# Performance work log

Hardware: AMD Instinct MI355X
Metric: run time of the kernel (lower is better)

Reference implementation:

```python
import jax, jax.numpy as jnp
import numpy as np

N = 50000
E = 800000
D_IN = 128
D_HID = 256


def setup_inputs() -> dict:
    key = jax.random.key(0)
    ks = jax.random.split(key, 12)
    s = 0.02
    return {
        "node_features": jax.random.normal(ks[0], (N, D_IN), dtype=jnp.float32),
        "edge_index": jax.random.randint(ks[1], (2, E), 0, N, dtype=jnp.int64),
        # layer 0 (input_dim -> hidden)
        "eps0": jnp.zeros((), dtype=jnp.float32),
        "W1_0": jax.random.normal(ks[2], (D_IN, D_HID), dtype=jnp.float32) * s,
        "b1_0": jnp.zeros((D_HID,), dtype=jnp.float32),
        "W2_0": jax.random.normal(ks[3], (D_HID, D_HID), dtype=jnp.float32) * s,
        "b2_0": jnp.zeros((D_HID,), dtype=jnp.float32),
        # layer 1 (hidden -> hidden)
        "eps1": jnp.zeros((), dtype=jnp.float32),
        "W1_1": jax.random.normal(ks[4], (D_HID, D_HID), dtype=jnp.float32) * s,
        "b1_1": jnp.zeros((D_HID,), dtype=jnp.float32),
        "W2_1": jax.random.normal(ks[5], (D_HID, D_HID), dtype=jnp.float32) * s,
        "b2_1": jnp.zeros((D_HID,), dtype=jnp.float32),
        # fc_out (hidden -> input_dim)
        "Wo": jax.random.normal(ks[6], (D_HID, D_IN), dtype=jnp.float32) * s,
        "bo": jnp.zeros((D_IN,), dtype=jnp.float32),
    }


def _gin_layer(x, src, dst, eps, W1, b1, W2, b2):
    # gather neighbor features + scatter-add into destination nodes
    agg = jnp.zeros_like(x).at[dst].add(x[src])  # [N, d]
    h = (1.0 + eps) * x + agg
    h = jax.nn.relu(h @ W1 + b1)
    return h @ W2 + b2


def reference(node_features, edge_index, eps0, W1_0, b1_0, W2_0, b2_0,
              eps1, W1_1, b1_1, W2_1, b2_1, Wo, bo):
    src, dst = edge_index[0], edge_index[1]
    h = _gin_layer(node_features, src, dst, eps0, W1_0, b1_0, W2_0, b2_0)
    h = _gin_layer(h, src, dst, eps1, W1_1, b1_1, W2_1, b2_1)
    return h @ Wo + bo  # [N, input_dim]
```

## Files before the change

### kernel.cpp

```cpp
#include <hip/hip_runtime.h>

#define NN 50000
#define NE 800000
#define DIN 128
#define DHID 256
#define MAXDEG 128

typedef __bf16 bf16x8 __attribute__((ext_vector_type(8)));
typedef float f32x4 __attribute__((ext_vector_type(4)));

static __device__ __forceinline__ unsigned short f2bf(float f) {
    unsigned u = __float_as_uint(f);
    unsigned r = 0x7fffu + ((u >> 16) & 1u);
    return (unsigned short)((u + r) >> 16);
}
static __device__ __forceinline__ float blo(unsigned u) { return __uint_as_float(u << 16); }
static __device__ __forceinline__ float bhi(unsigned u) { return __uint_as_float(u & 0xffff0000u); }


__global__ void bucket_kernel(const int* __restrict__ src, const int* __restrict__ dst,
                              int* __restrict__ cnt, int* __restrict__ srcs, int E) {
    int i4 = (blockIdx.x * blockDim.x + threadIdx.x) * 4;
    if (i4 >= E) return;
    int4 d4 = *(const int4*)&dst[i4];
    int4 s4 = *(const int4*)&src[i4];
    int t0 = atomicAdd(&cnt[d4.x], 1);
    int t1 = atomicAdd(&cnt[d4.y], 1);
    int t2 = atomicAdd(&cnt[d4.z], 1);
    int t3 = atomicAdd(&cnt[d4.w], 1);
    if (t0 < MAXDEG) srcs[(size_t)d4.x * MAXDEG + t0] = s4.x;
    if (t1 < MAXDEG) srcs[(size_t)d4.y * MAXDEG + t1] = s4.y;
    if (t2 < MAXDEG) srcs[(size_t)d4.z * MAXDEG + t2] = s4.z;
    if (t3 < MAXDEG) srcs[(size_t)d4.w * MAXDEG + t3] = s4.w;
}


__global__ void prep_kernel(const float* __restrict__ x, unsigned short* __restrict__ xb,
                            int* __restrict__ cnt,
                            const float* __restrict__ W1_0, const float* __restrict__ W2_0,
                            const float* __restrict__ W1_1, const float* __restrict__ W2_1,
                            const float* __restrict__ Wo,
                            unsigned short* __restrict__ w10t, unsigned short* __restrict__ w20t,
                            unsigned short* __restrict__ w11t, unsigned short* __restrict__ w21t,
                            unsigned short* __restrict__ wot) {
    int i = blockIdx.x * blockDim.x + threadIdx.x;
    if (i < NN) cnt[i] = 0;
    if (i < 262144) {
        const float* W; unsigned short* Wt; int K, N, idx;
        if (i < 32768)        { W = W1_0; Wt = w10t; K = 128; N = 256; idx = i; }
        else if (i < 98304)   { W = W2_0; Wt = w20t; K = 256; N = 256; idx = i - 32768; }
        else if (i < 163840)  { W = W1_1; Wt = w11t; K = 256; N = 256; idx = i - 98304; }
        else if (i < 229376)  { W = W2_1; Wt = w21t; K = 256; N = 256; idx = i - 163840; }
        else                  { W = Wo;   Wt = wot;  K = 256; N = 128; idx = i - 229376; }
        int k = idx / N;
        int n = idx - k * N;
        Wt[(size_t)n * K + k] = f2bf(W[idx]);
    }
    if (i * 4 < NN * DIN) {
        float4 v = *(const float4*)(x + (size_t)i * 4);
        ushort4 o;
        o.x = f2bf(v.x); o.y = f2bf(v.y); o.z = f2bf(v.z); o.w = f2bf(v.w);
        *(ushort4*)(xb + (size_t)i * 4) = o;
    }
}


template <int D>
__global__ void agg_bf16_kernel(const unsigned short* __restrict__ x, const int* __restrict__ cnt,
                                const int* __restrict__ srcs, const float* __restrict__ eps_p,
                                unsigned short* __restrict__ out, int n) {
    int gtid = blockIdx.x * blockDim.x + threadIdx.x;
    int node = gtid >> 6;
    int lane = threadIdx.x & 63;
    if (node >= n) return;
    int deg = cnt[node]; if (deg > MAXDEG) deg = MAXDEG;
    const int* sp = srcs + (size_t)node * MAXDEG;
    float e = 1.0f + eps_p[0];
    if constexpr (D == 128) {
        const unsigned* xp = (const unsigned*)x;
        float a0 = 0.f, a1 = 0.f, b0 = 0.f, b1 = 0.f;
        int i = 0;
        for (; i + 8 <= deg; i += 8) {
            unsigned v[8];
            #pragma unroll
            for (int j = 0; j < 8; j++) v[j] = xp[(size_t)sp[i + j] * 64 + lane];
            #pragma unroll
            for (int j = 0; j < 8; j += 2) {
                a0 += blo(v[j]);     a1 += bhi(v[j]);
                b0 += blo(v[j + 1]); b1 += bhi(v[j + 1]);
            }
        }
        for (; i < deg; i++) {
            unsigned v = xp[(size_t)sp[i] * 64 + lane];
            a0 += blo(v); a1 += bhi(v);
        }
        unsigned xv = xp[(size_t)node * 64 + lane];
        a0 += b0 + e * blo(xv);
        a1 += b1 + e * bhi(xv);
        ((unsigned*)out)[(size_t)node * 64 + lane] =
            (unsigned)f2bf(a0) | ((unsigned)f2bf(a1) << 16);
    } else {
        const uint2* xp = (const uint2*)x;
        float a0 = 0.f, a1 = 0.f, a2 = 0.f, a3 = 0.f;
        float b0 = 0.f, b1 = 0.f, b2 = 0.f, b3 = 0.f;
        int i = 0;
        for (; i + 8 <= deg; i += 8) {
            uint2 v[8];
            #pragma unroll
            for (int j = 0; j < 8; j++) v[j] = xp[(size_t)sp[i + j] * 64 + lane];
            #pragma unroll
            for (int j = 0; j < 8; j += 2) {
                a0 += blo(v[j].x);     a1 += bhi(v[j].x);     a2 += blo(v[j].y);     a3 += bhi(v[j].y);
                b0 += blo(v[j + 1].x); b1 += bhi(v[j + 1].x); b2 += blo(v[j + 1].y); b3 += bhi(v[j + 1].y);
            }
        }
        for (; i < deg; i++) {
            uint2 v = xp[(size_t)sp[i] * 64 + lane];
            a0 += blo(v.x); a1 += bhi(v.x); a2 += blo(v.y); a3 += bhi(v.y);
        }
        uint2 xv = xp[(size_t)node * 64 + lane];
        a0 += b0 + e * blo(xv.x);
        a1 += b1 + e * bhi(xv.x);
        a2 += b2 + e * blo(xv.y);
        a3 += b3 + e * bhi(xv.y);
        uint2 o;
        o.x = (unsigned)f2bf(a0) | ((unsigned)f2bf(a1) << 16);
        o.y = (unsigned)f2bf(a2) | ((unsigned)f2bf(a3) << 16);
        ((uint2*)out)[(size_t)node * 64 + lane] = o;
    }
}


template <int K1, int THREE>
__global__ __launch_bounds__(256, 2) void mlp_fused(
        const unsigned short* __restrict__ A,
        const unsigned short* __restrict__ W1t, const float* __restrict__ b1,
        const unsigned short* __restrict__ W2t, const float* __restrict__ b2,
        const unsigned short* __restrict__ W3t, const float* __restrict__ b3,
        unsigned short* __restrict__ Cb, float* __restrict__ Cf, int M) {
    constexpr int NKS1 = K1 / 32;
    __shared__ __align__(16) unsigned short H[(THREE ? 2 : 1) * 64 * 256];
    unsigned short* H1 = H;
    unsigned short* H2 = H + 64 * 256;

    const int tid = threadIdx.x;
    const int lane = tid & 63;
    const int w = tid >> 6;
    const int quad = lane >> 4;
    const int l16 = lane & 15;
    const size_t rowbase = (size_t)blockIdx.x * 64;

    bf16x8 bfrag[8][4];
    f32x4 bvv[4];

    #pragma unroll
    for (int ks = 0; ks < NKS1; ks++)
        #pragma unroll
        for (int nt = 0; nt < 4; nt++)
            bfrag[ks][nt] = *(const bf16x8*)&W1t[(size_t)(w * 64 + nt * 16 + l16) * K1 + ks * 32 + quad * 8];
    #pragma unroll
    for (int nt = 0; nt < 4; nt++)
        bvv[nt] = *(const f32x4*)&b1[w * 64 + nt * 16 + quad * 4];

    #pragma unroll
    for (int j = 0; j < 4; j++) {
        const unsigned short* ar = A + (rowbase + j * 16 + l16) * K1 + quad * 8;
        bf16x8 af[NKS1];
        #pragma unroll
        for (int ks = 0; ks < NKS1; ks++) af[ks] = *(const bf16x8*)(ar + ks * 32);
        f32x4 acc[4];
        #pragma unroll
        for (int nt = 0; nt < 4; nt++) acc[nt] = (f32x4)(0.f);
        #pragma unroll
        for (int ks = 0; ks < NKS1; ks++)
            #pragma unroll
            for (int nt = 0; nt < 4; nt++)
                acc[nt] = __builtin_amdgcn_mfma_f32_16x16x32_bf16(bfrag[ks][nt], af[ks], acc[nt], 0, 0, 0);
        int r = j * 16 + l16;
        #pragma unroll
        for (int nt = 0; nt < 4; nt++) {
            f32x4 v = acc[nt] + bvv[nt];
            v[0] = fmaxf(v[0], 0.f); v[1] = fmaxf(v[1], 0.f);
            v[2] = fmaxf(v[2], 0.f); v[3] = fmaxf(v[3], 0.f);
            int c = w * 8 + nt * 2 + (quad >> 1);
            int cs = c ^ (r & 7);
            uint2 o;
            o.x = (unsigned)f2bf(v[0]) | ((unsigned)f2bf(v[1]) << 16);
            o.y = (unsigned)f2bf(v[2]) | ((unsigned)f2bf(v[3]) << 16);
            *(uint2*)&H1[r * 256 + cs * 8 + (quad & 1) * 4] = o;
        }
    }
    __syncthreads();

    #pragma unroll
    for (int ks = 0; ks < 8; ks++)
        #pragma unroll
        for (int nt = 0; nt < 4; nt++)
            bfrag[ks][nt] = *(const bf16x8*)&W2t[(size_t)(w * 64 + nt * 16 + l16) * 256 + ks * 32 + quad * 8];
    #pragma unroll
    for (int nt = 0; nt < 4; nt++)
        bvv[nt] = *(const f32x4*)&b2[w * 64 + nt * 16 + quad * 4];

    #pragma unroll
    for (int j = 0; j < 4; j++) {
        int r = j * 16 + l16;
        bf16x8 af[8];
        #pragma unroll
        for (int ks = 0; ks < 8; ks++) {
            int cs = (ks * 4 + quad) ^ (r & 7);
            af[ks] = *(const bf16x8*)&H1[r * 256 + cs * 8];
        }
        f32x4 acc[4];
        #pragma unroll
        for (int nt = 0; nt < 4; nt++) acc[nt] = (f32x4)(0.f);
        #pragma unroll
        for (int ks = 0; ks < 8; ks++)
            #pragma unroll
            for (int nt = 0; nt < 4; nt++)
                acc[nt] = __builtin_amdgcn_mfma_f32_16x16x32_bf16(bfrag[ks][nt], af[ks], acc[nt], 0, 0, 0);
        if constexpr (!THREE) {
            size_t gm = rowbase + j * 16 + l16;
            if (gm < (size_t)M) {
                #pragma unroll
                for (int nt = 0; nt < 4; nt++) {
                    f32x4 v = acc[nt] + bvv[nt];
                    uint2 o;
                    o.x = (unsigned)f2bf(v[0]) | ((unsigned)f2bf(v[1]) << 16);
                    o.y = (unsigned)f2bf(v[2]) | ((unsigned)f2bf(v[3]) << 16);
                    *(uint2*)&Cb[gm * 256 + w * 64 + nt * 16 + quad * 4] = o;
                }
            }
        } else {
            #pragma unroll
            for (int nt = 0; nt < 4; nt++) {
                f32x4 v = acc[nt] + bvv[nt];
                int c = w * 8 + nt * 2 + (quad >> 1);
                int cs = c ^ (r & 7);
                uint2 o;
                o.x = (unsigned)f2bf(v[0]) | ((unsigned)f2bf(v[1]) << 16);
                o.y = (unsigned)f2bf(v[2]) | ((unsigned)f2bf(v[3]) << 16);
                *(uint2*)&H2[r * 256 + cs * 8 + (quad & 1) * 4] = o;
            }
        }
    }

    if constexpr (THREE) {
        __syncthreads();
        #pragma unroll
        for (int ks = 0; ks < 8; ks++)
            #pragma unroll
            for (int nt = 0; nt < 2; nt++)
                bfrag[ks][nt] = *(const bf16x8*)&W3t[(size_t)(w * 32 + nt * 16 + l16) * 256 + ks * 32 + quad * 8];
        f32x4 bv3[2];
        #pragma unroll
        for (int nt = 0; nt < 2; nt++)
            bv3[nt] = *(const f32x4*)&b3[w * 32 + nt * 16 + quad * 4];

        #pragma unroll
        for (int j = 0; j < 4; j++) {
            int r = j * 16 + l16;
            bf16x8 af[8];
            #pragma unroll
            for (int ks = 0; ks < 8; ks++) {
                int cs = (ks * 4 + quad) ^ (r & 7);
                af[ks] = *(const bf16x8*)&H2[r * 256 + cs * 8];
            }
            f32x4 acc[2];
            #pragma unroll
            for (int nt = 0; nt < 2; nt++) acc[nt] = (f32x4)(0.f);
            #pragma unroll
            for (int ks = 0; ks < 8; ks++)
                #pragma unroll
                for (int nt = 0; nt < 2; nt++)
                    acc[nt] = __builtin_amdgcn_mfma_f32_16x16x32_bf16(bfrag[ks][nt], af[ks], acc[nt], 0, 0, 0);
            size_t gm = rowbase + j * 16 + l16;
            if (gm < (size_t)M) {
                #pragma unroll
                for (int nt = 0; nt < 2; nt++) {
                    f32x4 v = acc[nt] + bv3[nt];
                    *(f32x4*)&Cf[gm * 128 + w * 32 + nt * 16 + quad * 4] = v;
                }
            }
        }
    }
}


static inline size_t align256(size_t v) { return (v + 255) & ~(size_t)255; }

extern "C" void kernel_launch(void* const* d_in, const int* in_sizes, int n_in,
                              void* d_out, int out_size, void* d_ws, size_t ws_size,
                              hipStream_t stream) {
    const float* x        = (const float*)d_in[0];
    const int*   ei       = (const int*)d_in[1];
    const float* eps0     = (const float*)d_in[2];
    const float* W1_0     = (const float*)d_in[3];
    const float* b1_0     = (const float*)d_in[4];
    const float* W2_0     = (const float*)d_in[5];
    const float* b2_0     = (const float*)d_in[6];
    const float* eps1     = (const float*)d_in[7];
    const float* W1_1     = (const float*)d_in[8];
    const float* b1_1     = (const float*)d_in[9];
    const float* W2_1     = (const float*)d_in[10];
    const float* b2_1     = (const float*)d_in[11];
    const float* Wo       = (const float*)d_in[12];
    const float* bo       = (const float*)d_in[13];
    float* out            = (float*)d_out;

    const int* srcE = ei;
    const int* dstE = ei + NE;

    char* p = (char*)d_ws;
    size_t o = 0;
    int* cnt  = (int*)(p + o); o = align256(o + (size_t)NN * 4);
    int* srcs = (int*)(p + o); o = align256(o + (size_t)NN * MAXDEG * 4);
    unsigned short* xb   = (unsigned short*)(p + o); o = align256(o + (size_t)NN * DIN * 2);
    unsigned short* w10t = (unsigned short*)(p + o); o = align256(o + (size_t)DHID * DIN * 2);
    unsigned short* w20t = (unsigned short*)(p + o); o = align256(o + (size_t)DHID * DHID * 2);
    unsigned short* w11t = (unsigned short*)(p + o); o = align256(o + (size_t)DHID * DHID * 2);
    unsigned short* w21t = (unsigned short*)(p + o); o = align256(o + (size_t)DHID * DHID * 2);
    unsigned short* wot  = (unsigned short*)(p + o); o = align256(o + (size_t)DIN * DHID * 2);
    unsigned short* bufA = (unsigned short*)(p + o); o = align256(o + (size_t)NN * DHID * 2 + 65536);
    unsigned short* bufB = (unsigned short*)(p + o); o = align256(o + (size_t)NN * DHID * 2 + 65536);

    prep_kernel<<<(NN * DIN / 4 + 255) / 256, 256, 0, stream>>>(
        x, xb, cnt, W1_0, W2_0, W1_1, W2_1, Wo, w10t, w20t, w11t, w21t, wot);
    bucket_kernel<<<(NE / 4 + 255) / 256, 256, 0, stream>>>(srcE, dstE, cnt, srcs, NE);

    int aggBlocks = (NN * 64 + 255) / 256;
    int mlpBlocks = (NN + 63) / 64;

    agg_bf16_kernel<DIN><<<aggBlocks, 256, 0, stream>>>(xb, cnt, srcs, eps0, bufA, NN);
    mlp_fused<128, 0><<<mlpBlocks, 256, 0, stream>>>(
        bufA, w10t, b1_0, w20t, b2_0, nullptr, nullptr, bufB, nullptr, NN);

    agg_bf16_kernel<DHID><<<aggBlocks, 256, 0, stream>>>(bufB, cnt, srcs, eps1, bufA, NN);
    mlp_fused<256, 1><<<mlpBlocks, 256, 0, stream>>>(
        bufA, w11t, b1_1, w21t, b2_1, wot, bo, nullptr, out, NN);
}
```

Measured before the change: 348.2 us.

## Pack multiple nodes per wave in aggregation and restructure MLP loop order

The aggregation kernel now assigns 4 (D=128) or 2 (D=256) nodes per wave, with each lane loading 16-byte uint4 chunks and reading neighbour indices as int4. The fused MLP switches from preloading all weight fragments per layer to streaming weights per k-step into a 4x4 accumulator tile, reuses a single shared buffer for both hidden layers, and drops the occupancy hint from launch_bounds. The bucket kernel processes 8 edges per thread instead of 4. These changes aim to widen memory transactions and cut register pressure, at the cost of more lane divergence from uneven node degrees within a wave and extra barriers.

Measured after the change: 331.1 us. -4.9%, faster.

```diff
diff --git a/kernel.cpp b/kernel.cpp
--- a/kernel.cpp
+++ b/kernel.cpp
@@ -20,18 +20,28 @@
 
 __global__ void bucket_kernel(const int* __restrict__ src, const int* __restrict__ dst,
                               int* __restrict__ cnt, int* __restrict__ srcs, int E) {
-    int i4 = (blockIdx.x * blockDim.x + threadIdx.x) * 4;
-    if (i4 >= E) return;
-    int4 d4 = *(const int4*)&dst[i4];
-    int4 s4 = *(const int4*)&src[i4];
-    int t0 = atomicAdd(&cnt[d4.x], 1);
-    int t1 = atomicAdd(&cnt[d4.y], 1);
-    int t2 = atomicAdd(&cnt[d4.z], 1);
-    int t3 = atomicAdd(&cnt[d4.w], 1);
-    if (t0 < MAXDEG) srcs[(size_t)d4.x * MAXDEG + t0] = s4.x;
-    if (t1 < MAXDEG) srcs[(size_t)d4.y * MAXDEG + t1] = s4.y;
-    if (t2 < MAXDEG) srcs[(size_t)d4.z * MAXDEG + t2] = s4.z;
-    if (t3 < MAXDEG) srcs[(size_t)d4.w * MAXDEG + t3] = s4.w;
+    int i8 = (blockIdx.x * blockDim.x + threadIdx.x) * 8;
+    if (i8 >= E) return;
+    int4 da = *(const int4*)&dst[i8];
+    int4 db = *(const int4*)&dst[i8 + 4];
+    int4 sa = *(const int4*)&src[i8];
+    int4 sb = *(const int4*)&src[i8 + 4];
+    int t0 = atomicAdd(&cnt[da.x], 1);
+    int t1 = atomicAdd(&cnt[da.y], 1);
+    int t2 = atomicAdd(&cnt[da.z], 1);
+    int t3 = atomicAdd(&cnt[da.w], 1);
+    int t4 = atomicAdd(&cnt[db.x], 1);
+    int t5 = atomicAdd(&cnt[db.y], 1);
+    int t6 = atomicAdd(&cnt[db.z], 1);
+    int t7 = atomicAdd(&cnt[db.w], 1);
+    if (t0 < MAXDEG) srcs[(size_t)da.x * MAXDEG + t0] = sa.x;
+    if (t1 < MAXDEG) srcs[(size_t)da.y * MAXDEG + t1] = sa.y;
+    if (t2 < MAXDEG) srcs[(size_t)da.z * MAXDEG + t2] = sa.z;
+    if (t3 < MAXDEG) srcs[(size_t)da.w * MAXDEG + t3] = sa.w;
+    if (t4 < MAXDEG) srcs[(size_t)db.x * MAXDEG + t4] = sb.x;
+    if (t5 < MAXDEG) srcs[(size_t)db.y * MAXDEG + t5] = sb.y;
+    if (t6 < MAXDEG) srcs[(size_t)db.z * MAXDEG + t6] = sb.z;
+    if (t7 < MAXDEG) srcs[(size_t)db.w * MAXDEG + t7] = sb.w;
 }
 
 
@@ -69,215 +79,213 @@
 __global__ void agg_bf16_kernel(const unsigned short* __restrict__ x, const int* __restrict__ cnt,
                                 const int* __restrict__ srcs, const float* __restrict__ eps_p,
                                 unsigned short* __restrict__ out, int n) {
-    int gtid = blockIdx.x * blockDim.x + threadIdx.x;
-    int node = gtid >> 6;
+    constexpr int G = (D == 128) ? 4 : 2;
+    constexpr int L = 64 / G;
+    constexpr int RQ = D / 8;
+    int tid = blockIdx.x * blockDim.x + threadIdx.x;
+    int wid = tid >> 6;
     int lane = threadIdx.x & 63;
+    int group = lane / L;
+    int li = lane % L;
+    int node = wid * G + group;
     if (node >= n) return;
     int deg = cnt[node]; if (deg > MAXDEG) deg = MAXDEG;
     const int* sp = srcs + (size_t)node * MAXDEG;
+    const uint4* xp = (const uint4*)x;
     float e = 1.0f + eps_p[0];
-    if constexpr (D == 128) {
-        const unsigned* xp = (const unsigned*)x;
-        float a0 = 0.f, a1 = 0.f, b0 = 0.f, b1 = 0.f;
-        int i = 0;
-        for (; i + 8 <= deg; i += 8) {
-            unsigned v[8];
-            #pragma unroll
-            for (int j = 0; j < 8; j++) v[j] = xp[(size_t)sp[i + j] * 64 + lane];
-            #pragma unroll
-            for (int j = 0; j < 8; j += 2) {
-                a0 += blo(v[j]);     a1 += bhi(v[j]);
-                b0 += blo(v[j + 1]); b1 += bhi(v[j + 1]);
-            }
-        }
-        for (; i < deg; i++) {
-            unsigned v = xp[(size_t)sp[i] * 64 + lane];
-            a0 += blo(v); a1 += bhi(v);
-        }
-        unsigned xv = xp[(size_t)node * 64 + lane];
-        a0 += b0 + e * blo(xv);
-        a1 += b1 + e * bhi(xv);
-        ((unsigned*)out)[(size_t)node * 64 + lane] =
-            (unsigned)f2bf(a0) | ((unsigned)f2bf(a1) << 16);
-    } else {
-        const uint2* xp = (const uint2*)x;
-        float a0 = 0.f, a1 = 0.f, a2 = 0.f, a3 = 0.f;
-        float b0 = 0.f, b1 = 0.f, b2 = 0.f, b3 = 0.f;
-        int i = 0;
-        for (; i + 8 <= deg; i += 8) {
-            uint2 v[8];
-            #pragma unroll
-            for (int j = 0; j < 8; j++) v[j] = xp[(size_t)sp[i + j] * 64 + lane];
-            #pragma unroll
-            for (int j = 0; j < 8; j += 2) {
-                a0 += blo(v[j].x);     a1 += bhi(v[j].x);     a2 += blo(v[j].y);     a3 += bhi(v[j].y);
-                b0 += blo(v[j + 1].x); b1 += bhi(v[j + 1].x); b2 += blo(v[j + 1].y); b3 += bhi(v[j + 1].y);
-            }
-        }
-        for (; i < deg; i++) {
-            uint2 v = xp[(size_t)sp[i] * 64 + lane];
-            a0 += blo(v.x); a1 += bhi(v.x); a2 += blo(v.y); a3 += bhi(v.y);
-        }
-        uint2 xv = xp[(size_t)node * 64 + lane];
-        a0 += b0 + e * blo(xv.x);
-        a1 += b1 + e * bhi(xv.x);
-        a2 += b2 + e * blo(xv.y);
-        a3 += b3 + e * bhi(xv.y);
-        uint2 o;
-        o.x = (unsigned)f2bf(a0) | ((unsigned)f2bf(a1) << 16);
-        o.y = (unsigned)f2bf(a2) | ((unsigned)f2bf(a3) << 16);
-        ((uint2*)out)[(size_t)node * 64 + lane] = o;
-    }
+
+    float a[8], b[8];
+    #pragma unroll
+    for (int j = 0; j < 8; j++) { a[j] = 0.f; b[j] = 0.f; }
+
+    int i = 0;
+    for (; i + 4 <= deg; i += 4) {
+        int4 s = *(const int4*)&sp[i];
+        uint4 v0 = xp[(size_t)s.x * RQ + li];
+        uint4 v1 = xp[(size_t)s.y * RQ + li];
+        uint4 v2 = xp[(size_t)s.z * RQ + li];
+        uint4 v3 = xp[(size_t)s.w * RQ + li];
+        a[0] += blo(v0.x); a[1] += bhi(v0.x); a[2] += blo(v0.y); a[3] += bhi(v0.y);
+        a[4] += blo(v0.z); a[5] += bhi(v0.z); a[6] += blo(v0.w); a[7] += bhi(v0.w);
+        b[0] += blo(v1.x); b[1] += bhi(v1.x); b[2] += blo(v1.y); b[3] += bhi(v1.y);
+        b[4] += blo(v1.z); b[5] += bhi(v1.z); b[6] += blo(v1.w); b[7] += bhi(v1.w);
+        a[0] += blo(v2.x); a[1] += bhi(v2.x); a[2] += blo(v2.y); a[3] += bhi(v2.y);
+        a[4] += blo(v2.z); a[5] += bhi(v2.z); a[6] += blo(v2.w); a[7] += bhi(v2.w);
+        b[0] += blo(v3.x); b[1] += bhi(v3.x); b[2] += blo(v3.y); b[3] += bhi(v3.y);
+        b[4] += blo(v3.z); b[5] += bhi(v3.z); b[6] += blo(v3.w); b[7] += bhi(v3.w);
+    }
+    for (; i < deg; i++) {
+        uint4 v = xp[(size_t)sp[i] * RQ + li];
+        a[0] += blo(v.x); a[1] += bhi(v.x); a[2] += blo(v.y); a[3] += bhi(v.y);
+        a[4] += blo(v.z); a[5] += bhi(v.z); a[6] += blo(v.w); a[7] += bhi(v.w);
+    }
+    uint4 xv = xp[(size_t)node * RQ + li];
+    a[0] += b[0] + e * blo(xv.x); a[1] += b[1] + e * bhi(xv.x);
+    a[2] += b[2] + e * blo(xv.y); a[3] += b[3] + e * bhi(xv.y);
+    a[4] += b[4] + e * blo(xv.z); a[5] += b[5] + e * bhi(xv.z);
+    a[6] += b[6] + e * blo(xv.w); a[7] += b[7] + e * bhi(xv.w);
+    uint4 o;
+    o.x = (unsigned)f2bf(a[0]) | ((unsigned)f2bf(a[1]) << 16);
+    o.y = (unsigned)f2bf(a[2]) | ((unsigned)f2bf(a[3]) << 16);
+    o.z = (unsigned)f2bf(a[4]) | ((unsigned)f2bf(a[5]) << 16);
+    o.w = (unsigned)f2bf(a[6]) | ((unsigned)f2bf(a[7]) << 16);
+    ((uint4*)out)[(size_t)node * RQ + li] = o;
 }
 
 
 template <int K1, int THREE>
-__global__ __launch_bounds__(256, 2) void mlp_fused(
+__global__ __launch_bounds__(256) void mlp_fused(
         const unsigned short* __restrict__ A,
         const unsigned short* __restrict__ W1t, const float* __restrict__ b1,
         const unsigned short* __restrict__ W2t, const float* __restrict__ b2,
         const unsigned short* __restrict__ W3t, const float* __restrict__ b3,
         unsigned short* __restrict__ Cb, float* __restrict__ Cf, int M) {
     constexpr int NKS1 = K1 / 32;
-    __shared__ __align__(16) unsigned short H[(THREE ? 2 : 1) * 64 * 256];
-    unsigned short* H1 = H;
-    unsigned short* H2 = H + 64 * 256;
-
-    const int tid = threadIdx.x;
-    const int lane = tid & 63;
-    const int w = tid >> 6;
+    __shared__ __align__(16) unsigned short H[64 * 256];
+
+    const int lane = threadIdx.x & 63;
+    const int w = threadIdx.x >> 6;
     const int quad = lane >> 4;
     const int l16 = lane & 15;
     const size_t rowbase = (size_t)blockIdx.x * 64;
 
-    bf16x8 bfrag[8][4];
-    f32x4 bvv[4];
+    f32x4 acc[4][4];
 
     #pragma unroll
-    for (int ks = 0; ks < NKS1; ks++)
+    for (int j = 0; j < 4; j++)
+        #pragma unroll
+        for (int nt = 0; nt < 4; nt++) acc[j][nt] = (f32x4)(0.f);
+    #pragma unroll 2
+    for (int ks = 0; ks < NKS1; ks++) {
+        bf16x8 bw[4];
         #pragma unroll
         for (int nt = 0; nt < 4; nt++)
-            bfrag[ks][nt] = *(const bf16x8*)&W1t[(size_t)(w * 64 + nt * 16 + l16) * K1 + ks * 32 + quad * 8];
-    #pragma unroll
-    for (int nt = 0; nt < 4; nt++)
-        bvv[nt] = *(const f32x4*)&b1[w * 64 + nt * 16 + quad * 4];
-
-    #pragma unroll
-    for (int j = 0; j < 4; j++) {
-        const unsigned short* ar = A + (rowbase + j * 16 + l16) * K1 + quad * 8;
-        bf16x8 af[NKS1];
-        #pragma unroll
-        for (int ks = 0; ks < NKS1; ks++) af[ks] = *(const bf16x8*)(ar + ks * 32);
-        f32x4 acc[4];
-        #pragma unroll
-        for (int nt = 0; nt < 4; nt++) acc[nt] = (f32x4)(0.f);
-        #pragma unroll
-        for (int ks = 0; ks < NKS1; ks++)
+            bw[nt] = *(const bf16x8*)&W1t[(size_t)(w * 64 + nt * 16 + l16) * K1 + ks * 32 + quad * 8];
+        #pragma unroll
+        for (int j = 0; j < 4; j++) {
+            bf16x8 af = *(const bf16x8*)&A[(rowbase + j * 16 + l16) * K1 + ks * 32 + quad * 8];
             #pragma unroll
             for (int nt = 0; nt < 4; nt++)
-                acc[nt] = __builtin_amdgcn_mfma_f32_16x16x32_bf16(bfrag[ks][nt], af[ks], acc[nt], 0, 0, 0);
-        int r = j * 16 + l16;
-        #pragma unroll
-        for (int nt = 0; nt < 4; nt++) {
-            f32x4 v = acc[nt] + bvv[nt];
-            v[0] = fmaxf(v[0], 0.f); v[1] = fmaxf(v[1], 0.f);
-            v[2] = fmaxf(v[2], 0.f); v[3] = fmaxf(v[3], 0.f);
-            int c = w * 8 + nt * 2 + (quad >> 1);
-            int cs = c ^ (r & 7);
-            uint2 o;
-            o.x = (unsigned)f2bf(v[0]) | ((unsigned)f2bf(v[1]) << 16);
-            o.y = (unsigned)f2bf(v[2]) | ((unsigned)f2bf(v[3]) << 16);
-            *(uint2*)&H1[r * 256 + cs * 8 + (quad & 1) * 4] = o;
-        }
-    }
-    __syncthreads();
-
-    #pragma unroll
-    for (int ks = 0; ks < 8; ks++)
+                acc[j][nt] = __builtin_amdgcn_mfma_f32_16x16x32_bf16(bw[nt], af, acc[j][nt], 0, 0, 0);
+        }
+    }
+    {
+        f32x4 bvv[4];
         #pragma unroll
         for (int nt = 0; nt < 4; nt++)
-            bfrag[ks][nt] = *(const bf16x8*)&W2t[(size_t)(w * 64 + nt * 16 + l16) * 256 + ks * 32 + quad * 8];
-    #pragma unroll
-    for (int nt = 0; nt < 4; nt++)
-        bvv[nt] = *(const f32x4*)&b2[w * 64 + nt * 16 + quad * 4];
-
-    #pragma unroll
-    for (int j = 0; j < 4; j++) {
-        int r = j * 16 + l16;
-        bf16x8 af[8];
-        #pragma unroll
-        for (int ks = 0; ks < 8; ks++) {
-            int cs = (ks * 4 + quad) ^ (r & 7);
-            af[ks] = *(const bf16x8*)&H1[r * 256 + cs * 8];
-        }
-        f32x4 acc[4];
-        #pragma unroll
-        for (int nt = 0; nt < 4; nt++) acc[nt] = (f32x4)(0.f);
-        #pragma unroll
-        for (int ks = 0; ks < 8; ks++)
-            #pragma unroll
-            for (int nt = 0; nt < 4; nt++)
-                acc[nt] = __builtin_amdgcn_mfma_f32_16x16x32_bf16(bfrag[ks][nt], af[ks], acc[nt], 0, 0, 0);
-        if constexpr (!THREE) {
-            size_t gm = rowbase + j * 16 + l16;
-            if (gm < (size_t)M) {
-                #pragma unroll
-                for (int nt = 0; nt < 4; nt++) {
-                    f32x4 v = acc[nt] + bvv[nt];
-                    uint2 o;
-                    o.x = (unsigned)f2bf(v[0]) | ((unsigned)f2bf(v[1]) << 16);
-                    o.y = (unsigned)f2bf(v[2]) | ((unsigned)f2bf(v[3]) << 16);
-                    *(uint2*)&Cb[gm * 256 + w * 64 + nt * 16 + quad * 4] = o;
-                }
-            }
-        } else {
+            bvv[nt] = *(const f32x4*)&b1[w * 64 + nt * 16 + quad * 4];
+        #pragma unroll
+        for (int j = 0; j < 4; j++) {
+            int r = j * 16 + l16;
             #pragma unroll
             for (int nt = 0; nt < 4; nt++) {
-                f32x4 v = acc[nt] + bvv[nt];
+                f32x4 v = acc[j][nt] + bvv[nt];
+                v[0] = fmaxf(v[0], 0.f); v[1] = fmaxf(v[1], 0.f);
+                v[2] = fmaxf(v[2], 0.f); v[3] = fmaxf(v[3], 0.f);
                 int c = w * 8 + nt * 2 + (quad >> 1);
                 int cs = c ^ (r & 7);
                 uint2 o;
                 o.x = (unsigned)f2bf(v[0]) | ((unsigned)f2bf(v[1]) << 16);
                 o.y = (unsigned)f2bf(v[2]) | ((unsigned)f2bf(v[3]) << 16);
-                *(uint2*)&H2[r * 256 + cs * 8 + (quad & 1) * 4] = o;
-            }
+                *(uint2*)&H[r * 256 + cs * 8 + (quad & 1) * 4] = o;
+            }
+        }
+    }
+    __syncthreads();
+
+    #pragma unroll
+    for (int j = 0; j < 4; j++)
+        #pragma unroll
+        for (int nt = 0; nt < 4; nt++) acc[j][nt] = (f32x4)(0.f);
+    #pragma unroll 2
+    for (int ks = 0; ks < 8; ks++) {
+        bf16x8 bw[4];
+        #pragma unroll
+        for (int nt = 0; nt < 4; nt++)
+            bw[nt] = *(const bf16x8*)&W2t[(size_t)(w * 64 + nt * 16 + l16) * 256 + ks * 32 + quad * 8];
+        #pragma unroll
+        for (int j = 0; j < 4; j++) {
+            int r = j * 16 + l16;
+            int cs = (ks * 4 + quad) ^ (r & 7);
+            bf16x8 af = *(const bf16x8*)&H[r * 256 + cs * 8];
+            #pragma unroll
+            for (int nt = 0; nt < 4; nt++)
+                acc[j][nt] = __builtin_amdgcn_mfma_f32_16x16x32_bf16(bw[nt], af, acc[j][nt], 0, 0, 0);
+        }
+    }
+    {
+        f32x4 bvv[4];
+        #pragma unroll
+        for (int nt = 0; nt < 4; nt++)
+            bvv[nt] = *(const f32x4*)&b2[w * 64 + nt * 16 + quad * 4];
+        if constexpr (!THREE) {
+            #pragma unroll
+            for (int j = 0; j < 4; j++) {
+                size_t gm = rowbase + j * 16 + l16;
+                if (gm < (size_t)M) {
+                    #pragma unroll
+                    for (int nt = 0; nt < 4; nt++) {
+                        f32x4 v = acc[j][nt] + bvv[nt];
+                        uint2 o;
+                        o.x = (unsigned)f2bf(v[0]) | ((unsigned)f2bf(v[1]) << 16);
+                        o.y = (unsigned)f2bf(v[2]) | ((unsigned)f2bf(v[3]) << 16);
+                        *(uint2*)&Cb[gm * 256 + w * 64 + nt * 16 + quad * 4] = o;
+                    }
+                }
+            }
+        } else {
+            __syncthreads();
+            #pragma unroll
+            for (int j = 0; j < 4; j++) {
+                int r = j * 16 + l16;
+                #pragma unroll
+                for (int nt = 0; nt < 4; nt++) {
+                    f32x4 v = acc[j][nt] + bvv[nt];
+                    int c = w * 8 + nt * 2 + (quad >> 1);
+                    int cs = c ^ (r & 7);
+                    uint2 o;
+                    o.x = (unsigned)f2bf(v[0]) | ((unsigned)f2bf(v[1]) << 16);
+                    o.y = (unsigned)f2bf(v[2]) | ((unsigned)f2bf(v[3]) << 16);
+                    *(uint2*)&H[r * 256 + cs * 8 + (quad & 1) * 4] = o;
+                }
+            }
+            __syncthreads();
         }
     }
 
     if constexpr (THREE) {
-        __syncthreads();
-        #pragma unroll
-        for (int ks = 0; ks < 8; ks++)
+        f32x4 acc3[4][2];
+        #pragma unroll
+        for (int j = 0; j < 4; j++)
+            #pragma unroll
+            for (int nt = 0; nt < 2; nt++) acc3[j][nt] = (f32x4)(0.f);
+        #pragma unroll 2
+        for (int ks = 0; ks < 8; ks++) {
+            bf16x8 bw[2];
             #pragma unroll
             for (int nt = 0; nt < 2; nt++)
-                bfrag[ks][nt] = *(const bf16x8*)&W3t[(size_t)(w * 32 + nt * 16 + l16) * 256 + ks * 32 + quad * 8];
+                bw[nt] = *(const bf16x8*)&W3t[(size_t)(w * 32 + nt * 16 + l16) * 256 + ks * 32 + quad * 8];
+            #pragma unroll
+            for (int j = 0; j < 4; j++) {
+                int r = j * 16 + l16;
+                int cs = (ks * 4 + quad) ^ (r & 7);
+                bf16x8 af = *(const bf16x8*)&H[r * 256 + cs * 8];
+                #pragma unroll
+                for (int nt = 0; nt < 2; nt++)
+                    acc3[j][nt] = __builtin_amdgcn_mfma_f32_16x16x32_bf16(bw[nt], af, acc3[j][nt], 0, 0, 0);
+            }
+        }
         f32x4 bv3[2];
         #pragma unroll
         for (int nt = 0; nt < 2; nt++)
             bv3[nt] = *(const f32x4*)&b3[w * 32 + nt * 16 + quad * 4];
-
         #pragma unroll
         for (int j = 0; j < 4; j++) {
-            int r = j * 16 + l16;
-            bf16x8 af[8];
-            #pragma unroll
-            for (int ks = 0; ks < 8; ks++) {
-                int cs = (ks * 4 + quad) ^ (r & 7);
-                af[ks] = *(const bf16x8*)&H2[r * 256 + cs * 8];
-            }
-            f32x4 acc[2];
-            #pragma unroll
-            for (int nt = 0; nt < 2; nt++) acc[nt] = (f32x4)(0.f);
-            #pragma unroll
-            for (int ks = 0; ks < 8; ks++)
-                #pragma unroll
-                for (int nt = 0; nt < 2; nt++)
-                    acc[nt] = __builtin_amdgcn_mfma_f32_16x16x32_bf16(bfrag[ks][nt], af[ks], acc[nt], 0, 0, 0);
             size_t gm = rowbase + j * 16 + l16;
             if (gm < (size_t)M) {
                 #pragma unroll
                 for (int nt = 0; nt < 2; nt++) {
-                    f32x4 v = acc[nt] + bv3[nt];
+                    f32x4 v = acc3[j][nt] + bv3[nt];
                     *(f32x4*)&Cf[gm * 128 + w * 32 + nt * 16 + quad * 4] = v;
                 }
             }
@@ -325,16 +333,17 @@
 
     prep_kernel<<<(NN * DIN / 4 + 255) / 256, 256, 0, stream>>>(
         x, xb, cnt, W1_0, W2_0, W1_1, W2_1, Wo, w10t, w20t, w11t, w21t, wot);
-    bucket_kernel<<<(NE / 4 + 255) / 256, 256, 0, stream>>>(srcE, dstE, cnt, srcs, NE);
-
-    int aggBlocks = (NN * 64 + 255) / 256;
+    bucket_kernel<<<(NE / 8 + 255) / 256, 256, 0, stream>>>(srcE, dstE, cnt, srcs, NE);
+
+    int aggBlocks128 = ((NN + 3) / 4 + 3) / 4;
+    int aggBlocks256 = ((NN + 1) / 2 + 3) / 4;
     int mlpBlocks = (NN + 63) / 64;
 
-    agg_bf16_kernel<DIN><<<aggBlocks, 256, 0, stream>>>(xb, cnt, srcs, eps0, bufA, NN);
+    agg_bf16_kernel<DIN><<<aggBlocks128, 256, 0, stream>>>(xb, cnt, srcs, eps0, bufA, NN);
     mlp_fused<128, 0><<<mlpBlocks, 256, 0, stream>>>(
         bufA, w10t, b1_0, w20t, b2_0, nullptr, nullptr, bufB, nullptr, NN);
 
-    agg_bf16_kernel<DHID><<<aggBlocks, 256, 0, stream>>>(bufB, cnt, srcs, eps1, bufA, NN);
+    agg_bf16_kernel<DHID><<<aggBlocks256, 256, 0, stream>>>(bufB, cnt, srcs, eps1, bufA, NN);
     mlp_fused<256, 1><<<mlpBlocks, 256, 0, stream>>>(
         bufA, w11t, b1_1, w21t, b2_1, wot, bo, nullptr, out, NN);
 }
```
